# Performance work log

Measured on AMD Instinct MI355X. Metric: run time of the kernel, lower is better.

## Reference

```python
import jax, jax.numpy as jnp
import numpy as np

LAMB = 0.01       # self.lamb
CASCADES = 3

# Forward difference D along `axis` with zero last row: (Dv)[i] = v[i+1]-v[i], (Dv)[N-1]=0.
# This is exactly the sparse matvec matmul(Dx, v.view(-1)).reshape(v.shape), batched.
def fwd_diff(v, axis):
    d = jnp.diff(v, axis=axis)
    pad = [(0, 0)] * v.ndim
    pad[axis] = (0, 1)
    return jnp.pad(d, pad)

# Exact adjoint D^T: (D^T p)[0] = -p[0]; (D^T p)[j] = p[j-1]-p[j]; (D^T p)[N-1] = p[N-2].
def fwd_diff_t(p, axis):
    n = p.shape[axis]
    pad_front = [(0, 0)] * p.ndim
    pad_front[axis] = (1, 0)
    a = jax.lax.slice_in_dim(jnp.pad(p, pad_front), 0, n, axis=axis)   # a[j] = p[j-1], a[0]=0
    pad_back = [(0, 0)] * p.ndim
    pad_back[axis] = (0, 1)
    b = jnp.pad(jax.lax.slice_in_dim(p, 0, n - 1, axis=axis), pad_back)  # b[j]=p[j], b[N-1]=0
    return a - b

def dual_prox(x, sig):
    # Dual AE block: clip onto [-sigma, sigma] ball (TV dual proximal)
    return jnp.clip(x, -sig, sig)

def setup_inputs() -> dict:
    key = jax.random.key(0)
    k1, k2 = jax.random.split(key)
    B, D, H, W = 2, 256, 256, 128
    image = jax.random.normal(k1, (B, D, H, W), dtype=jnp.float32)
    sino = jax.random.normal(k2, (B, D, H, W), dtype=jnp.float32)
    sigma = jnp.ones((4,), dtype=jnp.float32)
    nt = jnp.zeros((CASCADES,), dtype=jnp.float32)
    return {"image": image, "sino": sino, "sigma": sigma, "nt": nt}

def reference(image, sino, sigma, nt):
    t = image
    outs = [t]
    p = jnp.zeros_like(image)
    q = jnp.zeros_like(image)
    s = jnp.zeros_like(image)
    for c in range(CASCADES):
        # ITE (BeijingGeometry stand-in): data-fidelity gradient step
        z = t - LAMB * (t - sino)
        pnew = dual_prox(p - fwd_diff(z, 1), sigma[0])
        qnew = dual_prox(q - fwd_diff(z, 2), sigma[1])
        snew = dual_prox(s - fwd_diff(z, 3), sigma[2])
        znew = dual_prox(z, sigma[3])
        # momentum extrapolation
        p = pnew + nt[c] * (pnew - p)
        q = qnew + nt[c] * (qnew - q)
        s = snew + nt[c] * (snew - s)
        # divergence via adjoint stencils + primal update
        t = fwd_diff_t(p, 1) + fwd_diff_t(q, 2) + fwd_diff_t(s, 3) + znew
        outs.append(t)
    return tuple(outs)
```

## Files before the change

### kernel.cpp

```cpp
#include <hip/hip_runtime.h>

#define LAMB 0.01f
constexpr int Bc = 2, Dc = 256, Hc = 256, Wc = 128;
constexpr int HW  = Hc * Wc;
constexpr int NELEM_I = Bc * Dc * Hc * Wc;
constexpr int NBLK = NELEM_I / 1024;

__device__ __forceinline__ float clipf(float x, float s) {
    return fminf(fmaxf(x, -s), s);
}
__device__ __forceinline__ float dual_up(float pold, float dz, float sg, float ntc) {
    float pn = clipf(pold - dz, sg);
    return pn + ntc * (pn - pold);
}
__device__ __forceinline__ float zof(float t, float s) { return t + LAMB * (s - t); }

__device__ __forceinline__ void z4(const float* __restrict__ t,
                                   const float* __restrict__ s,
                                   int i, float* out) {
    float4 a = *(const float4*)(t + i);
    float4 b = *(const float4*)(s + i);
    out[0] = zof(a.x, b.x); out[1] = zof(a.y, b.y);
    out[2] = zof(a.z, b.z); out[3] = zof(a.w, b.w);
}

template <bool FIRST, bool WRITE_PQS, bool WRITE_COPY>
__global__ __launch_bounds__(256) void cascade_v4(
    const float* __restrict__ t_in, const float* __restrict__ sino,
    const float* __restrict__ p_in, const float* __restrict__ q_in,
    const float* __restrict__ s_in,
    float* __restrict__ p_out, float* __restrict__ q_out, float* __restrict__ s_out,
    float* __restrict__ t_out, float* __restrict__ copy_out,
    const float* __restrict__ sigma, const float* __restrict__ nt, int c)
{
    const int lb = (int)(blockIdx.x & 7) * (NBLK >> 3) + (int)(blockIdx.x >> 3);
    const int i0 = (lb * 256 + (int)threadIdx.x) * 4;

    const int w0 = i0 & (Wc - 1);
    const int h  = (i0 >> 7) & (Hc - 1);
    const int d  = (i0 >> 15) & (Dc - 1);

    const float s0 = sigma[0], s1 = sigma[1], s2 = sigma[2], s3 = sigma[3];
    const float ntc = nt[c];

    const float4 tc4 = *(const float4*)(t_in + i0);
    const float4 sn4 = *(const float4*)(sino + i0);
    if (WRITE_COPY) *(float4*)(copy_out + i0) = tc4;

    float zc[6];
    zc[1] = zof(tc4.x, sn4.x); zc[2] = zof(tc4.y, sn4.y);
    zc[3] = zof(tc4.z, sn4.z); zc[4] = zof(tc4.w, sn4.w);
    zc[0] = (w0 > 0)      ? zof(t_in[i0 - 1], sino[i0 - 1]) : 0.f;
    zc[5] = (w0 < Wc - 4) ? zof(t_in[i0 + 4], sino[i0 + 4]) : 0.f;

    float zhp[4] = {0,0,0,0}, zhm[4] = {0,0,0,0};
    float zdp[4] = {0,0,0,0}, zdm[4] = {0,0,0,0};
    const bool hlast = (h == Hc - 1), dlast = (d == Dc - 1);
    if (!hlast) z4(t_in, sino, i0 + Wc, zhp);
    if (h > 0)  z4(t_in, sino, i0 - Wc, zhm);
    if (!dlast) z4(t_in, sino, i0 + HW, zdp);
    if (d > 0)  z4(t_in, sino, i0 - HW, zdm);

    float pc[4], pm[4] = {0,0,0,0}, dt1[4];
    {
        float4 pv = FIRST ? make_float4(0,0,0,0) : *(const float4*)(p_in + i0);
        float po[4] = {pv.x, pv.y, pv.z, pv.w};
#pragma unroll
        for (int k = 0; k < 4; ++k)
            pc[k] = dual_up(po[k], dlast ? 0.f : (zdp[k] - zc[k + 1]), s0, ntc);
        if (d > 0) {
            float4 pmv = FIRST ? make_float4(0,0,0,0) : *(const float4*)(p_in + i0 - HW);
            float pom[4] = {pmv.x, pmv.y, pmv.z, pmv.w};
#pragma unroll
            for (int k = 0; k < 4; ++k)
                pm[k] = dual_up(pom[k], zc[k + 1] - zdm[k], s0, ntc);
        }
#pragma unroll
        for (int k = 0; k < 4; ++k)
            dt1[k] = pm[k] - (dlast ? 0.f : pc[k]);
    }

    float qc[4], qm[4] = {0,0,0,0}, dt2[4];
    {
        float4 qv = FIRST ? make_float4(0,0,0,0) : *(const float4*)(q_in + i0);
        float qo[4] = {qv.x, qv.y, qv.z, qv.w};
#pragma unroll
        for (int k = 0; k < 4; ++k)
            qc[k] = dual_up(qo[k], hlast ? 0.f : (zhp[k] - zc[k + 1]), s1, ntc);
        if (h > 0) {
            float4 qmv = FIRST ? make_float4(0,0,0,0) : *(const float4*)(q_in + i0 - Wc);
            float qom[4] = {qmv.x, qmv.y, qmv.z, qmv.w};
#pragma unroll
            for (int k = 0; k < 4; ++k)
                qm[k] = dual_up(qom[k], zc[k + 1] - zhm[k], s1, ntc);
        }
#pragma unroll
        for (int k = 0; k < 4; ++k)
            dt2[k] = qm[k] - (hlast ? 0.f : qc[k]);
    }

    float sc[4], dt3[4];
    {
        float4 sv = FIRST ? make_float4(0,0,0,0) : *(const float4*)(s_in + i0);
        float so[4] = {sv.x, sv.y, sv.z, sv.w};
#pragma unroll
        for (int k = 0; k < 4; ++k) {
            const bool wlast = (w0 + k == Wc - 1);
            sc[k] = dual_up(so[k], wlast ? 0.f : (zc[k + 2] - zc[k + 1]), s2, ntc);
        }
        float smv = 0.f;
        if (w0 > 0) {
            float som = FIRST ? 0.f : s_in[i0 - 1];
            smv = dual_up(som, zc[1] - zc[0], s2, ntc);
        }
        dt3[0] = smv - sc[0];
#pragma unroll
        for (int k = 1; k < 4; ++k)
            dt3[k] = sc[k - 1] - ((w0 + k == Wc - 1) ? 0.f : sc[k]);
    }

    if (WRITE_PQS) {
        *(float4*)(p_out + i0) = make_float4(pc[0], pc[1], pc[2], pc[3]);
        *(float4*)(q_out + i0) = make_float4(qc[0], qc[1], qc[2], qc[3]);
        *(float4*)(s_out + i0) = make_float4(sc[0], sc[1], sc[2], sc[3]);
    }
    float4 tn;
    tn.x = dt1[0] + dt2[0] + dt3[0] + clipf(zc[1], s3);
    tn.y = dt1[1] + dt2[1] + dt3[1] + clipf(zc[2], s3);
    tn.z = dt1[2] + dt2[2] + dt3[2] + clipf(zc[3], s3);
    tn.w = dt1[3] + dt2[3] + dt3[3] + clipf(zc[4], s3);
    *(float4*)(t_out + i0) = tn;
}

template <bool FIRST, bool WRITE_COPY>
__global__ __launch_bounds__(256) void dual_kernel(
    const float* __restrict__ t_in, const float* __restrict__ sino,
    float* p, float* q, float* s,
    float* __restrict__ copy_out,
    const float* __restrict__ sigma, const float* __restrict__ nt, int c)
{
    const int idx = blockIdx.x * blockDim.x + threadIdx.x;
    if (idx >= NELEM_I) return;
    const int w = idx & (Wc - 1);
    const int h = (idx >> 7) & (Hc - 1);
    const int d = (idx >> 15) & (Dc - 1);

    const float s0 = sigma[0], s1 = sigma[1], s2 = sigma[2];
    const float ntc = nt[c];

    const float tc = t_in[idx];
    const float zc = zof(tc, sino[idx]);
    if (WRITE_COPY) copy_out[idx] = tc;
    auto Z = [&](int i) { return zof(t_in[i], sino[i]); };

    float pold = FIRST ? 0.f : p[idx];
    float qold = FIRST ? 0.f : q[idx];
    float sold = FIRST ? 0.f : s[idx];
    p[idx] = dual_up(pold, (d < Dc - 1) ? (Z(idx + HW) - zc) : 0.f, s0, ntc);
    q[idx] = dual_up(qold, (h < Hc - 1) ? (Z(idx + Wc) - zc) : 0.f, s1, ntc);
    s[idx] = dual_up(sold, (w < Wc - 1) ? (Z(idx + 1) - zc) : 0.f, s2, ntc);
}

__global__ __launch_bounds__(256) void primal_kernel(
    const float* __restrict__ t_in, const float* __restrict__ sino,
    const float* __restrict__ p, const float* __restrict__ q,
    const float* __restrict__ s,
    float* __restrict__ t_out, const float* __restrict__ sigma)
{
    const int idx = blockIdx.x * blockDim.x + threadIdx.x;
    if (idx >= NELEM_I) return;
    const int w = idx & (Wc - 1);
    const int h = (idx >> 7) & (Hc - 1);
    const int d = (idx >> 15) & (Dc - 1);

    const float zc = zof(t_in[idx], sino[idx]);

    float dt1 = ((d > 0) ? p[idx - HW] : 0.f) - ((d < Dc - 1) ? p[idx] : 0.f);
    float dt2 = ((h > 0) ? q[idx - Wc] : 0.f) - ((h < Hc - 1) ? q[idx] : 0.f);
    float dt3 = ((w > 0) ? s[idx - 1] : 0.f) - ((w < Wc - 1) ? s[idx] : 0.f);

    t_out[idx] = dt1 + dt2 + dt3 + clipf(zc, sigma[3]);
}

extern "C" void kernel_launch(void* const* d_in, const int* in_sizes, int n_in,
                              void* d_out, int out_size, void* d_ws, size_t ws_size,
                              hipStream_t stream) {
    const float* image = (const float*)d_in[0];
    const float* sino  = (const float*)d_in[1];
    const float* sigma = (const float*)d_in[2];
    const float* nt    = (const float*)d_in[3];

    float* out  = (float*)d_out;
    float* out0 = out;
    float* out1 = out + (size_t)NELEM_I;
    float* out2 = out + 2 * (size_t)NELEM_I;
    float* out3 = out + 3 * (size_t)NELEM_I;

    const size_t ARR = (size_t)NELEM_I * sizeof(float);

    if (ws_size >= 6 * ARR) {
        float* pA = (float*)d_ws;
        float* qA = pA + NELEM_I;
        float* sA = qA + NELEM_I;
        float* pB = sA + NELEM_I;
        float* qB = pB + NELEM_I;
        float* sB = qB + NELEM_I;

        dim3 block(256), grid(NBLK);
        cascade_v4<true, true, true><<<grid, block, 0, stream>>>(
            image, sino, nullptr, nullptr, nullptr, pA, qA, sA, out1, out0, sigma, nt, 0);
        cascade_v4<false, true, false><<<grid, block, 0, stream>>>(
            out1, sino, pA, qA, sA, pB, qB, sB, out2, nullptr, sigma, nt, 1);
        cascade_v4<false, false, false><<<grid, block, 0, stream>>>(
            out2, sino, pB, qB, sB, nullptr, nullptr, nullptr, out3, nullptr, sigma, nt, 2);
    } else {
        float* p = (float*)d_ws;
        float* q = p + NELEM_I;
        float* s = q + NELEM_I;

        dim3 block(256), grid(NELEM_I / 256);
        dual_kernel<true, true><<<grid, block, 0, stream>>>(image, sino, p, q, s, out0, sigma, nt, 0);
        primal_kernel<<<grid, block, 0, stream>>>(image, sino, p, q, s, out1, sigma);
        dual_kernel<false, false><<<grid, block, 0, stream>>>(out1, sino, p, q, s, nullptr, sigma, nt, 1);
        primal_kernel<<<grid, block, 0, stream>>>(out1, sino, p, q, s, out2, sigma);
        dual_kernel<false, false><<<grid, block, 0, stream>>>(out2, sino, p, q, s, nullptr, sigma, nt, 2);
        primal_kernel<<<grid, block, 0, stream>>>(out2, sino, p, q, s, out3, sigma);
    }
}
```

Measured before the change: 668.9 us.

## Fuse all three cascades into one halo-tiled kernel with LDS-resident state

Replaces the three per-cascade kernels with one kernel. Each block loads an 8x8x32 tile plus a 3-cell halo of z into LDS and keeps p, q, s and z in LDS across all three cascades, recomputing the shrinking halo redundantly. This removes the global round trips of p/q/s and the intermediate t reads between cascades. In exchange it does redundant halo compute, uses about 125 KiB of LDS per block so occupancy is low, and writes outputs with scalar nontemporal stores.

```diff
diff --git a/kernel.cpp b/kernel.cpp
--- a/kernel.cpp
+++ b/kernel.cpp
@@ -2,184 +2,175 @@
 
 #define LAMB 0.01f
 constexpr int Bc = 2, Dc = 256, Hc = 256, Wc = 128;
-constexpr int HW  = Hc * Wc;
-constexpr int NELEM_I = Bc * Dc * Hc * Wc;
-constexpr int NBLK = NELEM_I / 1024;
+constexpr int HWc = Hc * Wc;
+constexpr int NELEM = Bc * Dc * HWc;
+
+constexpr int TD = 8, TH = 8, TW = 32;
+constexpr int RD = TD + 6, RH = TH + 6, RW = TW + 6;
+constexpr int RWP = 40;
+constexpr int NROWS = RD * RH;
+constexpr int NTHR = 1024;
+constexpr int GDt = Dc / TD, GHt = Hc / TH, GWt = Wc / TW;
+constexpr int NBLK = Bc * GDt * GHt * GWt;
+
+static_assert(4 * NROWS * RWP * 4 <= 160 * 1024, "LDS over 160 KiB");
+static_assert(NBLK % 8 == 0, "swizzle needs nblk % 8 == 0");
+
+typedef float f4 __attribute__((ext_vector_type(4)));
 
 __device__ __forceinline__ float clipf(float x, float s) {
     return fminf(fmaxf(x, -s), s);
 }
+__device__ __forceinline__ float zof(float t, float s) { return t + LAMB * (s - t); }
 __device__ __forceinline__ float dual_up(float pold, float dz, float sg, float ntc) {
     float pn = clipf(pold - dz, sg);
     return pn + ntc * (pn - pold);
 }
-__device__ __forceinline__ float zof(float t, float s) { return t + LAMB * (s - t); }
 
-__device__ __forceinline__ void z4(const float* __restrict__ t,
-                                   const float* __restrict__ s,
-                                   int i, float* out) {
-    float4 a = *(const float4*)(t + i);
-    float4 b = *(const float4*)(s + i);
-    out[0] = zof(a.x, b.x); out[1] = zof(a.y, b.y);
-    out[2] = zof(a.z, b.z); out[3] = zof(a.w, b.w);
-}
+__global__ __launch_bounds__(NTHR) void fused3(
+    const float* __restrict__ image, const float* __restrict__ sino,
+    float* __restrict__ out0, float* __restrict__ out1,
+    float* __restrict__ out2, float* __restrict__ out3,
+    const float* __restrict__ sigma, const float* __restrict__ nt)
+{
+    __shared__ float Z[NROWS * RWP];
+    __shared__ float P[NROWS * RWP];
+    __shared__ float Q[NROWS * RWP];
+    __shared__ float S[NROWS * RWP];
 
-template <bool FIRST, bool WRITE_PQS, bool WRITE_COPY>
-__global__ __launch_bounds__(256) void cascade_v4(
-    const float* __restrict__ t_in, const float* __restrict__ sino,
-    const float* __restrict__ p_in, const float* __restrict__ q_in,
-    const float* __restrict__ s_in,
-    float* __restrict__ p_out, float* __restrict__ q_out, float* __restrict__ s_out,
-    float* __restrict__ t_out, float* __restrict__ copy_out,
-    const float* __restrict__ sigma, const float* __restrict__ nt, int c)
-{
-    const int lb = (int)(blockIdx.x & 7) * (NBLK >> 3) + (int)(blockIdx.x >> 3);
-    const int i0 = (lb * 256 + (int)threadIdx.x) * 4;
-
-    const int w0 = i0 & (Wc - 1);
-    const int h  = (i0 >> 7) & (Hc - 1);
-    const int d  = (i0 >> 15) & (Dc - 1);
+    int bid = (int)blockIdx.x;
+    bid = (bid & 7) * (NBLK >> 3) + (bid >> 3);
+    const int wT = bid & (GWt - 1);
+    const int hT = (bid >> 2) & (GHt - 1);
+    const int dT = (bid >> 7) & (GDt - 1);
+    const int b  = bid >> 12;
+    const int d0 = dT * TD, h0 = hT * TH, w0 = wT * TW;
+    const int base = b * Dc * HWc;
 
     const float s0 = sigma[0], s1 = sigma[1], s2 = sigma[2], s3 = sigma[3];
-    const float ntc = nt[c];
+    const int tid = (int)threadIdx.x;
 
-    const float4 tc4 = *(const float4*)(t_in + i0);
-    const float4 sn4 = *(const float4*)(sino + i0);
-    if (WRITE_COPY) *(float4*)(copy_out + i0) = tc4;
-
-    float zc[6];
-    zc[1] = zof(tc4.x, sn4.x); zc[2] = zof(tc4.y, sn4.y);
-    zc[3] = zof(tc4.z, sn4.z); zc[4] = zof(tc4.w, sn4.w);
-    zc[0] = (w0 > 0)      ? zof(t_in[i0 - 1], sino[i0 - 1]) : 0.f;
-    zc[5] = (w0 < Wc - 4) ? zof(t_in[i0 + 4], sino[i0 + 4]) : 0.f;
-
-    float zhp[4] = {0,0,0,0}, zhm[4] = {0,0,0,0};
-    float zdp[4] = {0,0,0,0}, zdm[4] = {0,0,0,0};
-    const bool hlast = (h == Hc - 1), dlast = (d == Dc - 1);
-    if (!hlast) z4(t_in, sino, i0 + Wc, zhp);
-    if (h > 0)  z4(t_in, sino, i0 - Wc, zhm);
-    if (!dlast) z4(t_in, sino, i0 + HW, zdp);
-    if (d > 0)  z4(t_in, sino, i0 - HW, zdm);
-
-    float pc[4], pm[4] = {0,0,0,0}, dt1[4];
-    {
-        float4 pv = FIRST ? make_float4(0,0,0,0) : *(const float4*)(p_in + i0);
-        float po[4] = {pv.x, pv.y, pv.z, pv.w};
-#pragma unroll
-        for (int k = 0; k < 4; ++k)
-            pc[k] = dual_up(po[k], dlast ? 0.f : (zdp[k] - zc[k + 1]), s0, ntc);
-        if (d > 0) {
-            float4 pmv = FIRST ? make_float4(0,0,0,0) : *(const float4*)(p_in + i0 - HW);
-            float pom[4] = {pmv.x, pmv.y, pmv.z, pmv.w};
-#pragma unroll
-            for (int k = 0; k < 4; ++k)
-                pm[k] = dual_up(pom[k], zc[k + 1] - zdm[k], s0, ntc);
-        }
-#pragma unroll
-        for (int k = 0; k < 4; ++k)
-            dt1[k] = pm[k] - (dlast ? 0.f : pc[k]);
-    }
-
-    float qc[4], qm[4] = {0,0,0,0}, dt2[4];
-    {
-        float4 qv = FIRST ? make_float4(0,0,0,0) : *(const float4*)(q_in + i0);
-        float qo[4] = {qv.x, qv.y, qv.z, qv.w};
-#pragma unroll
-        for (int k = 0; k < 4; ++k)
-            qc[k] = dual_up(qo[k], hlast ? 0.f : (zhp[k] - zc[k + 1]), s1, ntc);
-        if (h > 0) {
-            float4 qmv = FIRST ? make_float4(0,0,0,0) : *(const float4*)(q_in + i0 - Wc);
-            float qom[4] = {qmv.x, qmv.y, qmv.z, qmv.w};
-#pragma unroll
-            for (int k = 0; k < 4; ++k)
-                qm[k] = dual_up(qom[k], zc[k + 1] - zhm[k], s1, ntc);
-        }
-#pragma unroll
-        for (int k = 0; k < 4; ++k)
-            dt2[k] = qm[k] - (hlast ? 0.f : qc[k]);
-    }
-
-    float sc[4], dt3[4];
-    {
-        float4 sv = FIRST ? make_float4(0,0,0,0) : *(const float4*)(s_in + i0);
-        float so[4] = {sv.x, sv.y, sv.z, sv.w};
+    for (int t = tid; t < NROWS * 10; t += NTHR) {
+        const int row = t / 10, g = t - row * 10;
+        const int rd = row / RH, rh = row - rd * RH;
+        const int gd = d0 - 3 + rd, gh = h0 - 3 + rh;
+        const bool rowok = ((unsigned)gd < (unsigned)Dc) && ((unsigned)gh < (unsigned)Hc);
+        const int rbase = base + gd * HWc + gh * Wc;
+        f4 z;
 #pragma unroll
         for (int k = 0; k < 4; ++k) {
-            const bool wlast = (w0 + k == Wc - 1);
-            sc[k] = dual_up(so[k], wlast ? 0.f : (zc[k + 2] - zc[k + 1]), s2, ntc);
+            const int gw = w0 - 3 + g * 4 + k;
+            float v = 0.f;
+            if (rowok && (unsigned)gw < (unsigned)Wc) {
+                const int gix = rbase + gw;
+                v = zof(image[gix], sino[gix]);
+            }
+            z[k] = v;
         }
-        float smv = 0.f;
-        if (w0 > 0) {
-            float som = FIRST ? 0.f : s_in[i0 - 1];
-            smv = dual_up(som, zc[1] - zc[0], s2, ntc);
+        *(f4*)&Z[row * RWP + g * 4] = z;
+    }
+    for (int t = tid; t < TD * TH * (TW / 4); t += NTHR) {
+        const int g = t & (TW / 4 - 1);
+        const int r = t >> 3;
+        const int td = r >> 3, th = r & 7;
+        const int gix = base + (d0 + td) * HWc + (h0 + th) * Wc + w0 + g * 4;
+        __builtin_nontemporal_store(*(const f4*)&image[gix], (f4*)&out0[gix]);
+    }
+    __syncthreads();
+
+#pragma unroll
+    for (int c = 0; c < 3; ++c) {
+        const float ntc = nt[c];
+
+        for (int t = tid; t < 169 * 10; t += NTHR) {
+            const int row13 = t / 10, g = t - row13 * 10;
+            const int rd = row13 / 13, rh = row13 - (row13 / 13) * 13;
+            const int li = (rd * RH + rh) * RWP + g * 4;
+
+            const f4 zc4 = *(const f4*)&Z[li];
+            const float z5 = (g < 9) ? Z[li + 4] : 0.f;
+            const f4 zd4 = *(const f4*)&Z[li + RH * RWP];
+            const f4 zh4 = *(const f4*)&Z[li + RWP];
+
+            f4 po = {0.f, 0.f, 0.f, 0.f}, qo = po, so = po;
+            if (c > 0) {
+                po = *(const f4*)&P[li];
+                qo = *(const f4*)&Q[li];
+                so = *(const f4*)&S[li];
+            }
+            const int gd = d0 - 3 + rd, gh = h0 - 3 + rh;
+            const bool dok = (unsigned)gd < (unsigned)Dc;
+            const bool hok = (unsigned)gh < (unsigned)Hc;
+            const bool dlast = (gd == Dc - 1), hlast = (gh == Hc - 1);
+
+            f4 pn, qn, sn;
+#pragma unroll
+            for (int k = 0; k < 4; ++k) {
+                const int gw = w0 - 3 + g * 4 + k;
+                const bool inb = dok && hok && ((unsigned)gw < (unsigned)Wc);
+                const float zck = zc4[k];
+                const float zr  = (k == 3) ? z5 : zc4[k + 1];
+                const float dzD = dlast ? 0.f : (zd4[k] - zck);
+                const float dzH = hlast ? 0.f : (zh4[k] - zck);
+                const float dzW = (gw == Wc - 1) ? 0.f : (zr - zck);
+                pn[k] = inb ? dual_up(po[k], dzD, s0, ntc) : 0.f;
+                qn[k] = inb ? dual_up(qo[k], dzH, s1, ntc) : 0.f;
+                sn[k] = inb ? dual_up(so[k], dzW, s2, ntc) : 0.f;
+            }
+            *(f4*)&P[li] = pn;
+            *(f4*)&Q[li] = qn;
+            *(f4*)&S[li] = sn;
         }
-        dt3[0] = smv - sc[0];
+        __syncthreads();
+
+        float* outc = (c == 0) ? out1 : ((c == 1) ? out2 : out3);
+        for (int t = tid; t < 144 * 10; t += NTHR) {
+            const int row12 = t / 10, g = t - row12 * 10;
+            const int rdm = row12 / 12;
+            const int rd = 1 + rdm, rh = 1 + (row12 - rdm * 12);
+            const int li = (rd * RH + rh) * RWP + g * 4;
+
+            const f4 pc = *(const f4*)&P[li];
+            const f4 pm = *(const f4*)&P[li - RH * RWP];
+            const f4 qc = *(const f4*)&Q[li];
+            const f4 qm = *(const f4*)&Q[li - RWP];
+            const f4 sc = *(const f4*)&S[li];
+            const float sm1 = S[li - 1];
+            const f4 zc4 = *(const f4*)&Z[li];
+
+            float tn[4];
 #pragma unroll
-        for (int k = 1; k < 4; ++k)
-            dt3[k] = sc[k - 1] - ((w0 + k == Wc - 1) ? 0.f : sc[k]);
+            for (int k = 0; k < 4; ++k) {
+                const float smk = (k == 0) ? sm1 : sc[k - 1];
+                tn[k] = (pm[k] - pc[k]) + (qm[k] - qc[k]) + (smk - sc[k])
+                      + clipf(zc4[k], s3);
+            }
+
+            const int gd = d0 - 3 + rd, gh = h0 - 3 + rh;
+            const int rix = base + gd * HWc + gh * Wc;
+            const bool tilerow = (rd >= 3 && rd < 3 + TD && rh >= 3 && rh < 3 + TH);
+            if (tilerow) {
+#pragma unroll
+                for (int k = 0; k < 4; ++k) {
+                    const int rw = g * 4 + k;
+                    if (rw >= 3 && rw < 3 + TW)
+                        __builtin_nontemporal_store(tn[k], &outc[rix + (w0 - 3 + rw)]);
+                }
+            }
+            if (c < 2) {
+                const bool dhok = ((unsigned)gd < (unsigned)Dc) && ((unsigned)gh < (unsigned)Hc);
+                f4 zn;
+#pragma unroll
+                for (int k = 0; k < 4; ++k) {
+                    const int gw = w0 - 3 + g * 4 + k;
+                    const bool inb = dhok && ((unsigned)gw < (unsigned)Wc);
+                    zn[k] = inb ? zof(tn[k], sino[rix + gw]) : 0.f;
+                }
+                *(f4*)&Z[li] = zn;
+            }
+        }
+        __syncthreads();
     }
-
-    if (WRITE_PQS) {
-        *(float4*)(p_out + i0) = make_float4(pc[0], pc[1], pc[2], pc[3]);
-        *(float4*)(q_out + i0) = make_float4(qc[0], qc[1], qc[2], qc[3]);
-        *(float4*)(s_out + i0) = make_float4(sc[0], sc[1], sc[2], sc[3]);
-    }
-    float4 tn;
-    tn.x = dt1[0] + dt2[0] + dt3[0] + clipf(zc[1], s3);
-    tn.y = dt1[1] + dt2[1] + dt3[1] + clipf(zc[2], s3);
-    tn.z = dt1[2] + dt2[2] + dt3[2] + clipf(zc[3], s3);
-    tn.w = dt1[3] + dt2[3] + dt3[3] + clipf(zc[4], s3);
-    *(float4*)(t_out + i0) = tn;
-}
-
-template <bool FIRST, bool WRITE_COPY>
-__global__ __launch_bounds__(256) void dual_kernel(
-    const float* __restrict__ t_in, const float* __restrict__ sino,
-    float* p, float* q, float* s,
-    float* __restrict__ copy_out,
-    const float* __restrict__ sigma, const float* __restrict__ nt, int c)
-{
-    const int idx = blockIdx.x * blockDim.x + threadIdx.x;
-    if (idx >= NELEM_I) return;
-    const int w = idx & (Wc - 1);
-    const int h = (idx >> 7) & (Hc - 1);
-    const int d = (idx >> 15) & (Dc - 1);
-
-    const float s0 = sigma[0], s1 = sigma[1], s2 = sigma[2];
-    const float ntc = nt[c];
-
-    const float tc = t_in[idx];
-    const float zc = zof(tc, sino[idx]);
-    if (WRITE_COPY) copy_out[idx] = tc;
-    auto Z = [&](int i) { return zof(t_in[i], sino[i]); };
-
-    float pold = FIRST ? 0.f : p[idx];
-    float qold = FIRST ? 0.f : q[idx];
-    float sold = FIRST ? 0.f : s[idx];
-    p[idx] = dual_up(pold, (d < Dc - 1) ? (Z(idx + HW) - zc) : 0.f, s0, ntc);
-    q[idx] = dual_up(qold, (h < Hc - 1) ? (Z(idx + Wc) - zc) : 0.f, s1, ntc);
-    s[idx] = dual_up(sold, (w < Wc - 1) ? (Z(idx + 1) - zc) : 0.f, s2, ntc);
-}
-
-__global__ __launch_bounds__(256) void primal_kernel(
-    const float* __restrict__ t_in, const float* __restrict__ sino,
-    const float* __restrict__ p, const float* __restrict__ q,
-    const float* __restrict__ s,
-    float* __restrict__ t_out, const float* __restrict__ sigma)
-{
-    const int idx = blockIdx.x * blockDim.x + threadIdx.x;
-    if (idx >= NELEM_I) return;
-    const int w = idx & (Wc - 1);
-    const int h = (idx >> 7) & (Hc - 1);
-    const int d = (idx >> 15) & (Dc - 1);
-
-    const float zc = zof(t_in[idx], sino[idx]);
-
-    float dt1 = ((d > 0) ? p[idx - HW] : 0.f) - ((d < Dc - 1) ? p[idx] : 0.f);
-    float dt2 = ((h > 0) ? q[idx - Wc] : 0.f) - ((h < Hc - 1) ? q[idx] : 0.f);
-    float dt3 = ((w > 0) ? s[idx - 1] : 0.f) - ((w < Wc - 1) ? s[idx] : 0.f);
-
-    t_out[idx] = dt1 + dt2 + dt3 + clipf(zc, sigma[3]);
 }
 
 extern "C" void kernel_launch(void* const* d_in, const int* in_sizes, int n_in,
@@ -191,39 +182,8 @@
     const float* nt    = (const float*)d_in[3];
 
     float* out  = (float*)d_out;
-    float* out0 = out;
-    float* out1 = out + (size_t)NELEM_I;
-    float* out2 = out + 2 * (size_t)NELEM_I;
-    float* out3 = out + 3 * (size_t)NELEM_I;
-
-    const size_t ARR = (size_t)NELEM_I * sizeof(float);
-
-    if (ws_size >= 6 * ARR) {
-        float* pA = (float*)d_ws;
-        float* qA = pA + NELEM_I;
-        float* sA = qA + NELEM_I;
-        float* pB = sA + NELEM_I;
-        float* qB = pB + NELEM_I;
-        float* sB = qB + NELEM_I;
-
-        dim3 block(256), grid(NBLK);
-        cascade_v4<true, true, true><<<grid, block, 0, stream>>>(
-            image, sino, nullptr, nullptr, nullptr, pA, qA, sA, out1, out0, sigma, nt, 0);
-        cascade_v4<false, true, false><<<grid, block, 0, stream>>>(
-            out1, sino, pA, qA, sA, pB, qB, sB, out2, nullptr, sigma, nt, 1);
-        cascade_v4<false, false, false><<<grid, block, 0, stream>>>(
-            out2, sino, pB, qB, sB, nullptr, nullptr, nullptr, out3, nullptr, sigma, nt, 2);
-    } else {
-        float* p = (float*)d_ws;
-        float* q = p + NELEM_I;
-        float* s = q + NELEM_I;
-
-        dim3 block(256), grid(NELEM_I / 256);
-        dual_kernel<true, true><<<grid, block, 0, stream>>>(image, sino, p, q, s, out0, sigma, nt, 0);
-        primal_kernel<<<grid, block, 0, stream>>>(image, sino, p, q, s, out1, sigma);
-        dual_kernel<false, false><<<grid, block, 0, stream>>>(out1, sino, p, q, s, nullptr, sigma, nt, 1);
-        primal_kernel<<<grid, block, 0, stream>>>(out1, sino, p, q, s, out2, sigma);
-        dual_kernel<false, false><<<grid, block, 0, stream>>>(out2, sino, p, q, s, nullptr, sigma, nt, 2);
-        primal_kernel<<<grid, block, 0, stream>>>(out2, sino, p, q, s, out3, sigma);
-    }
+    fused3<<<dim3(NBLK), dim3(NTHR), 0, stream>>>(
+        image, sino,
+        out, out + (size_t)NELEM, out + 2 * (size_t)NELEM, out + 3 * (size_t)NELEM,
+        sigma, nt);
 }
```

After: 722.5 us. +8.0%, slower.
